# Optimization experiments

Hardware: AMD Instinct MI355X
Metric: run time of the kernel (lower is better)

The kernel has to match this reference:

```python
import jax, jax.numpy as jnp
import numpy as np

# FP4 E2M1 constants (from the torch module)
EXP_BITS = 2
EXP_BIAS = 1          # 2**(EXP_BITS-1) - 1
MANT_BITS = 1
MAX_EXP_FIELD = 3     # (1 << EXP_BITS) - 1
MIN_NORMAL_EXP = 0    # 1 - EXP_BIAS
FP4_MAX = 6.0         # (1 + 1/2) * 2**(MAX_EXP_FIELD-1 - EXP_BIAS + 1) = 1.5 * 4
GROUP = 128


def fp4_quant_dequant(x):
    """Faithful composition of _float_to_fp4 followed by _fp4_to_float (E2M1,
    subnormal-aware), expressed in float arithmetic (bit pack/unpack cancels)."""
    a = jnp.abs(x)
    zero_mask = a == 0
    a_safe = jnp.where(zero_mask, jnp.float32(1e-8), a)
    e = jnp.floor(jnp.log2(a_safe))                      # unbiased exponent
    is_sub = e < MIN_NORMAL_EXP
    e_c = jnp.clip(e, MIN_NORMAL_EXP, MAX_EXP_FIELD - EXP_BIAS)
    mant_scale = float(1 << MANT_BITS)                   # 2.0
    mant_normal = jnp.clip(jnp.round((a_safe / jnp.exp2(e_c) - 1.0) * mant_scale), 0.0, mant_scale - 1.0)
    mant_sub = jnp.clip(jnp.round(a_safe / (2.0 ** MIN_NORMAL_EXP) * mant_scale), 0.0, mant_scale - 1.0)
    mant = jnp.where(is_sub, mant_sub, mant_normal)
    # decode (_fp4_to_float): normals (1 + m/2)*2^(e), subnormals (m/2)*2^(1-bias)
    val_normal = (1.0 + mant / mant_scale) * jnp.exp2(e_c)
    val_sub = (mant / mant_scale) * (2.0 ** (1 - EXP_BIAS))
    val = jnp.where(is_sub, val_sub, val_normal)
    val = jnp.where(x < 0, -val, val)
    return jnp.where(zero_mask, jnp.zeros_like(val), val)


def setup_inputs() -> dict:
    key = jax.random.key(0)
    k1, k2, k3 = jax.random.split(key, 3)
    x = jax.random.normal(k1, (4096, 4096), dtype=jnp.float32)
    weight = jax.random.normal(k2, (4096, 4096), dtype=jnp.float32) * 0.02
    b = jax.random.normal(k3, (4096,), dtype=jnp.float32)
    return {"x": x, "weight": weight, "b": b}


def reference(x, weight, b):
    out_f, in_f = weight.shape
    wg = weight.reshape(out_f, in_f // GROUP, GROUP)
    amax = jnp.max(jnp.abs(wg), axis=-1, keepdims=True)       # [out, groups, 1]
    scale = jnp.where(amax == 0, jnp.float32(1.0), amax / FP4_MAX)
    w_deq = (fp4_quant_dequant(wg / scale) * scale).reshape(out_f, in_f)
    return x @ w_deq.T + b
```

## Files before the change

### kernel.cpp

```cpp
#include <hip/hip_runtime.h>
#include <hip/hip_bf16.h>
#include <stdint.h>

#define KDIM 4096
#define NDIM 4096
#define MDIM 4096
#define BM 256
#define BN 256
#define BK 64

typedef __attribute__((ext_vector_type(8))) short bf16x8;
typedef __attribute__((ext_vector_type(4))) float f32x4;


__device__ __forceinline__ unsigned short bf16bits(float f) {
    union { float f; uint32_t u; } c; c.f = f;
    uint32_t u = c.u;
    uint32_t r = (u + 0x7fffu + ((u >> 16) & 1u)) >> 16;
    return (unsigned short)r;
}

__device__ __forceinline__ float fp4qd(float x) {
    float a = fabsf(x);
    if (a == 0.0f) return 0.0f;
    float e = floorf(log2f(a));
    float val;
    if (e < 0.0f) {
        float mant = fminf(fmaxf(rintf(a * 2.0f), 0.0f), 1.0f);
        val = mant * 0.5f;
    } else {
        float ec = fminf(e, 2.0f);
        float p  = exp2f(ec);
        float mant = fminf(fmaxf(rintf((a / p - 1.0f) * 2.0f), 0.0f), 1.0f);
        val = (1.0f + 0.5f * mant) * p;
    }
    return (x < 0.0f) ? -val : val;
}

__device__ __forceinline__ void gld16(void* lds, const void* g) {
    __builtin_amdgcn_global_load_lds(
        (const __attribute__((address_space(1))) unsigned int*)g,
        (__attribute__((address_space(3))) unsigned int*)lds,
        16, 0, 0);
}

__global__ __launch_bounds__(256) void prep_kernel(const float* __restrict__ X,
                                                   const float* __restrict__ W,
                                                   unsigned short* __restrict__ Xb,
                                                   unsigned short* __restrict__ Wq) {
    int bid = blockIdx.x;
    int tid = threadIdx.x;
    if (bid < 16384) {
        size_t i = ((size_t)bid * 256 + tid) * 4;
        float4 v = *(const float4*)(X + i);
        ushort4 o;
        o.x = bf16bits(v.x); o.y = bf16bits(v.y);
        o.z = bf16bits(v.z); o.w = bf16bits(v.w);
        *(ushort4*)(Xb + i) = o;
    } else {
        size_t base = ((size_t)(bid - 16384) * 256 + tid) * 4;
        float4 v = *(const float4*)(W + base);
        float am = fmaxf(fmaxf(fabsf(v.x), fabsf(v.y)),
                         fmaxf(fabsf(v.z), fabsf(v.w)));
        #pragma unroll
        for (int s = 16; s; s >>= 1) am = fmaxf(am, __shfl_xor(am, s));
        float scale = (am == 0.0f) ? 1.0f : am / 6.0f;
        ushort4 o;
        o.x = bf16bits(fp4qd(v.x / scale) * scale);
        o.y = bf16bits(fp4qd(v.y / scale) * scale);
        o.z = bf16bits(fp4qd(v.z / scale) * scale);
        o.w = bf16bits(fp4qd(v.w / scale) * scale);
        *(ushort4*)(Wq + base) = o;
    }
}


#define BAR()    __builtin_amdgcn_s_barrier()
#define LGKM(n)  asm volatile("s_waitcnt lgkmcnt(" #n ")" ::: "memory")
#define VM0()    asm volatile("s_waitcnt vmcnt(0)" ::: "memory")
#define SCH0()   __builtin_amdgcn_sched_barrier(0)
#define PRIO(x)  __builtin_amdgcn_s_setprio(x)

__global__ __launch_bounds__(512, 2) void gemm256(const unsigned short* __restrict__ A,
                                                  const unsigned short* __restrict__ B,
                                                  const float* __restrict__ bias,
                                                  float* __restrict__ C) {
    __shared__ __attribute__((aligned(16))) char smem[2][2][2][16384];
    char* sm = (char*)&smem[0][0][0][0];

    const int t = threadIdx.x;
    const int l = t & 63;
    const int w = __builtin_amdgcn_readfirstlane(t >> 6);
    const int wm = w >> 2;
    const int wn = w & 3;

    int bid = blockIdx.x;
    int swz = (bid & 7) * 32 + (bid >> 3);
    int brow = (swz >> 4) * BM;
    int bcol = (swz & 15) * BN;

    const int lr8  = l >> 3;
    const int slot = l & 7;
    const int scol = (slot ^ lr8) << 3;
    const unsigned short* pA = A + (size_t)(brow + w * 8 + lr8) * KDIM + scol;
    const unsigned short* pB = B + (size_t)(bcol + w * 8 + lr8) * KDIM + scol;

#define STAGE(b, op, h, kt) do {                                               \
    const unsigned short* _s = ((op) ? pB : pA)                                \
        + (size_t)(h) * 128 * KDIM + (size_t)(kt) * BK;                        \
    gld16(sm + (b) * 65536 + (op) * 32768 + (h) * 16384 + w * 1024, _s);       \
    gld16(sm + (b) * 65536 + (op) * 32768 + (h) * 16384 + 8192 + w * 1024,     \
          _s + (size_t)64 * KDIM);                                             \
} while (0)

    const int fr  = l & 15;
    const int fq  = l >> 4;
    const int kx0 = ((fq    ) ^ (fr & 7)) << 4;
    const int kx1 = ((fq + 4) ^ (fr & 7)) << 4;
    const int frA = fr * 128;

#define RD_A(b, mh, arr) do {                                                   \
    const char* _p = sm + (b) * 65536 + wm * 16384 + (mh) * 8192 + frA;         \
    _Pragma("unroll")                                                           \
    for (int m = 0; m < 4; ++m) {                                               \
        arr[m][0] = *(const bf16x8*)(_p + m * 2048 + kx0);                      \
        arr[m][1] = *(const bf16x8*)(_p + m * 2048 + kx1);                      \
    }                                                                           \
} while (0)

#define RD_B(b, nh, arr) do {                                                   \
    const char* _p = sm + (b) * 65536 + 32768 + wn * 8192 + (nh) * 4096 + frA;  \
    _Pragma("unroll")                                                           \
    for (int n = 0; n < 2; ++n) {                                               \
        arr[n][0] = *(const bf16x8*)(_p + n * 2048 + kx0);                      \
        arr[n][1] = *(const bf16x8*)(_p + n * 2048 + kx1);                      \
    }                                                                           \
} while (0)

#define MMG(mh, AV)                                                             \
    _Pragma("unroll")                                                           \
    for (int ks = 0; ks < 2; ++ks)                                              \
        _Pragma("unroll")                                                       \
        for (int m = 0; m < 4; ++m) {                                           \
            acc[(mh)*4+m][0] = __builtin_amdgcn_mfma_f32_16x16x32_bf16(         \
                AV[m][ks], bvA[0][ks], acc[(mh)*4+m][0], 0, 0, 0);              \
            acc[(mh)*4+m][1] = __builtin_amdgcn_mfma_f32_16x16x32_bf16(         \
                AV[m][ks], bvA[1][ks], acc[(mh)*4+m][1], 0, 0, 0);              \
            acc[(mh)*4+m][2] = __builtin_amdgcn_mfma_f32_16x16x32_bf16(         \
                AV[m][ks], bvB[0][ks], acc[(mh)*4+m][2], 0, 0, 0);              \
            acc[(mh)*4+m][3] = __builtin_amdgcn_mfma_f32_16x16x32_bf16(         \
                AV[m][ks], bvB[1][ks], acc[(mh)*4+m][3], 0, 0, 0);              \
        }

    f32x4 acc[8][4];
    #pragma unroll
    for (int m = 0; m < 8; ++m)
        #pragma unroll
        for (int n = 0; n < 4; ++n)
            acc[m][n] = f32x4{0.f, 0.f, 0.f, 0.f};

    bf16x8 avE[4][2], avO[4][2], bvA[2][2], bvB[2][2];

#define TILE_K(b, ktNext) do {                                                  \
    STAGE((b)^1, 0, 0, ktNext); STAGE((b)^1, 0, 1, ktNext);                     \
    STAGE((b)^1, 1, 0, ktNext); STAGE((b)^1, 1, 1, ktNext);                     \
    LGKM(8); SCH0();                                                            \
    PRIO(1); MMG(0, avE); PRIO(0);                                              \
    LGKM(0); SCH0();                                                            \
    VM0();                                                                      \
    BAR(); SCH0();                                                              \
    PRIO(1); MMG(1, avO); PRIO(0);                                              \
    RD_B((b)^1, 0, bvA); RD_B((b)^1, 1, bvB);                                   \
    RD_A((b)^1, 0, avE); RD_A((b)^1, 1, avO);                                   \
} while (0)

    STAGE(0, 0, 0, 0); STAGE(0, 0, 1, 0); STAGE(0, 1, 0, 0); STAGE(0, 1, 1, 0);
    VM0();
    BAR(); SCH0();
    RD_B(0, 0, bvA); RD_B(0, 1, bvB);
    RD_A(0, 0, avE); RD_A(0, 1, avO);

    for (int it = 0; it < 32; ++it) {
        const int k1 = 2 * it + 1;
        const int k2 = (2 * it + 2) & 63;
        TILE_K(0, k1);
        TILE_K(1, k2);
    }

    float bb[4];
    #pragma unroll
    for (int n = 0; n < 4; ++n) bb[n] = bias[bcol + wn * 64 + n * 16 + fr];
    #pragma unroll
    for (int mi = 0; mi < 8; ++mi) {
        #pragma unroll
        for (int q = 0; q < 4; ++q) {
            int row = brow + wm * 128 + mi * 16 + fq * 4 + q;
            float* crow = C + (size_t)row * NDIM + bcol + wn * 64;
            #pragma unroll
            for (int n = 0; n < 4; ++n)
                crow[n * 16 + fr] = acc[mi][n][q] + bb[n];
        }
    }
}

extern "C" void kernel_launch(void* const* d_in, const int* in_sizes, int n_in,
                              void* d_out, int out_size, void* d_ws, size_t ws_size,
                              hipStream_t stream) {
    const float* x = (const float*)d_in[0];
    const float* w = (const float*)d_in[1];
    const float* b = (const float*)d_in[2];
    float* out = (float*)d_out;

    unsigned short* xb = (unsigned short*)d_ws;
    unsigned short* wq = xb + (size_t)NDIM * KDIM;

    prep_kernel<<<32768, 256, 0, stream>>>(x, w, xb, wq);
    gemm256<<<(MDIM / BM) * (NDIM / BN), 512, 0, stream>>>(xb, wq, b, out);
}
```

Measured before the change: 149.9 us.

## Reschedule LDS fragment reads to overlap with MFMA in double-buffered K loop

Restructures the per-K-tile schedule of the bf16 GEMM main loop. B fragments become ping-pong register sets, so the next tile's B reads and first A half can be issued after the barrier and before the second MFMA group. The second A half is now read at the start of each tile instead of at the end of the previous one. This is meant to hide LDS read latency behind MFMA work, at the cost of extra registers for the duplicated B fragments and possible occupancy or spill pressure.

```diff
diff --git a/kernel.cpp b/kernel.cpp
--- a/kernel.cpp
+++ b/kernel.cpp
@@ -137,19 +137,19 @@
     }                                                                           \
 } while (0)
 
-#define MMG(mh, AV)                                                             \
+#define MMG(mh, AV, BA, BB)                                                     \
     _Pragma("unroll")                                                           \
     for (int ks = 0; ks < 2; ++ks)                                              \
         _Pragma("unroll")                                                       \
         for (int m = 0; m < 4; ++m) {                                           \
             acc[(mh)*4+m][0] = __builtin_amdgcn_mfma_f32_16x16x32_bf16(         \
-                AV[m][ks], bvA[0][ks], acc[(mh)*4+m][0], 0, 0, 0);              \
+                AV[m][ks], BA[0][ks], acc[(mh)*4+m][0], 0, 0, 0);               \
             acc[(mh)*4+m][1] = __builtin_amdgcn_mfma_f32_16x16x32_bf16(         \
-                AV[m][ks], bvA[1][ks], acc[(mh)*4+m][1], 0, 0, 0);              \
+                AV[m][ks], BA[1][ks], acc[(mh)*4+m][1], 0, 0, 0);               \
             acc[(mh)*4+m][2] = __builtin_amdgcn_mfma_f32_16x16x32_bf16(         \
-                AV[m][ks], bvB[0][ks], acc[(mh)*4+m][2], 0, 0, 0);              \
+                AV[m][ks], BB[0][ks], acc[(mh)*4+m][2], 0, 0, 0);               \
             acc[(mh)*4+m][3] = __builtin_amdgcn_mfma_f32_16x16x32_bf16(         \
-                AV[m][ks], bvB[1][ks], acc[(mh)*4+m][3], 0, 0, 0);              \
+                AV[m][ks], BB[1][ks], acc[(mh)*4+m][3], 0, 0, 0);               \
         }
 
     f32x4 acc[8][4];
@@ -159,32 +159,32 @@
         for (int n = 0; n < 4; ++n)
             acc[m][n] = f32x4{0.f, 0.f, 0.f, 0.f};
 
-    bf16x8 avE[4][2], avO[4][2], bvA[2][2], bvB[2][2];
-
-#define TILE_K(b, ktNext) do {                                                  \
-    STAGE((b)^1, 0, 0, ktNext); STAGE((b)^1, 0, 1, ktNext);                     \
-    STAGE((b)^1, 1, 0, ktNext); STAGE((b)^1, 1, 1, ktNext);                     \
+    bf16x8 avE[4][2], avO[4][2];
+    bf16x8 bvAe[2][2], bvBe[2][2], bvAo[2][2], bvBo[2][2];
+
+#define TILE_K(j, BAc, BBc, BAn, BBn, kNext) do {                               \
+                                                                     \
+    RD_A(j, 1, avO);                                                            \
+    STAGE((j)^1, 0, 0, kNext); STAGE((j)^1, 0, 1, kNext);                       \
+    STAGE((j)^1, 1, 0, kNext); STAGE((j)^1, 1, 1, kNext);                       \
     LGKM(8); SCH0();                                                            \
-    PRIO(1); MMG(0, avE); PRIO(0);                                              \
-    LGKM(0); SCH0();                                                            \
-    VM0();                                                                      \
-    BAR(); SCH0();                                                              \
-    PRIO(1); MMG(1, avO); PRIO(0);                                              \
-    RD_B((b)^1, 0, bvA); RD_B((b)^1, 1, bvB);                                   \
-    RD_A((b)^1, 0, avE); RD_A((b)^1, 1, avO);                                   \
+    PRIO(1); MMG(0, avE, BAc, BBc); PRIO(0);                                    \
+                                                                      \
+    LGKM(0); VM0(); BAR(); SCH0();                                              \
+    RD_B((j)^1, 0, BAn); RD_B((j)^1, 1, BBn); RD_A((j)^1, 0, avE);              \
+    PRIO(1); MMG(1, avO, BAc, BBc); PRIO(0);                                    \
 } while (0)
 
     STAGE(0, 0, 0, 0); STAGE(0, 0, 1, 0); STAGE(0, 1, 0, 0); STAGE(0, 1, 1, 0);
     VM0();
     BAR(); SCH0();
-    RD_B(0, 0, bvA); RD_B(0, 1, bvB);
-    RD_A(0, 0, avE); RD_A(0, 1, avO);
+    RD_B(0, 0, bvAe); RD_B(0, 1, bvBe); RD_A(0, 0, avE);
 
     for (int it = 0; it < 32; ++it) {
         const int k1 = 2 * it + 1;
         const int k2 = (2 * it + 2) & 63;
-        TILE_K(0, k1);
-        TILE_K(1, k2);
+        TILE_K(0, bvAe, bvBe, bvAo, bvBo, k1);
+        TILE_K(1, bvAo, bvBo, bvAe, bvBe, k2);
     }
 
     float bb[4];
```

Result: slower. 221.9 us (+48.0%).
